# Performance work log

Hardware: AMD Instinct MI355X
Metric: run time of the kernel (lower is better)

## Reference

```python
import jax, jax.numpy as jnp
import numpy as np

N_VERTS = 100000  # number of vertices
N_EDGES = 20000   # number of hyperedges
N_PAIRS = 800000  # (vertex, hyperedge) incidence pairs
DIM = 128
N_LAYERS = 3


def _segment_softmax(vals, seg, num_segments):
    # numerically stable softmax of per-pair values within each segment
    m = jax.ops.segment_max(vals, seg, num_segments=num_segments)
    ex = jnp.exp(vals - m[seg])
    s = jax.ops.segment_sum(ex, seg, num_segments=num_segments)
    return ex / s[seg]


def setup_inputs() -> dict:
    key = jax.random.key(0)
    k1, k2, k3, k4, k5, k6 = jax.random.split(key, 6)
    X = jax.random.normal(k1, (N_VERTS, DIM), dtype=jnp.float32)
    Ws = jax.random.normal(k2, (N_LAYERS, DIM, DIM), dtype=jnp.float32) * 0.05
    bs = jax.random.normal(k3, (N_LAYERS, DIM), dtype=jnp.float32) * 0.05
    e2v_weight = jax.random.uniform(k4, (N_PAIRS,), dtype=jnp.float32)
    pair_v = jax.random.randint(k5, (N_PAIRS,), 0, N_VERTS, dtype=jnp.int32)
    pair_e = jax.random.randint(k6, (N_PAIRS,), 0, N_EDGES, dtype=jnp.int32)
    return {"X": X, "Ws": Ws, "bs": bs, "e2v_weight": e2v_weight,
            "pair_v": pair_v, "pair_e": pair_e}


def reference(X, Ws, bs, e2v_weight, pair_v, pair_e):
    # v2e softmax weights: incidence values are all ones -> softmax per hyperedge
    ones = jnp.ones((pair_e.shape[0],), dtype=X.dtype)
    w_v2e = _segment_softmax(ones, pair_e, N_EDGES)            # [P]
    # e2v softmax weights: softmax of e2v_weight per destination vertex
    w_e2v = _segment_softmax(e2v_weight, pair_v, N_VERTS)      # [P]

    for l in range(N_LAYERS):
        X = X @ Ws[l] + bs[l]                                   # theta
        # v2e: vertex -> hyperedge softmax-weighted aggregation
        Xe = jax.ops.segment_sum(w_v2e[:, None] * X[pair_v], pair_e,
                                 num_segments=N_EDGES)          # [E, D]
        # e2v: hyperedge -> vertex softmax-weighted aggregation
        X = jax.ops.segment_sum(w_e2v[:, None] * Xe[pair_e], pair_v,
                                num_segments=N_VERTS)           # [N, D]
        X = jax.nn.relu(X)                                      # dropout = identity (eval)
    return X
```

## Files before the change

kernel.cpp:

```cpp
#include <hip/hip_runtime.h>
#include <hip/hip_fp16.h>

#define NV 100000
#define NE 20000
#define NP 800000
#define DIM 128
#define NEP 20032

#define EB_SH 7
#define EB 128
#define NBKE ((NE + EB - 1) / EB)
#define ECAP 8192
#define VB_SH 8
#define VB 256
#define NBKV ((NV + VB - 1) / VB)
#define VCAP 3072

#define PPB 8192
#define NPB ((NP + PPB - 1) / PPB)

typedef unsigned short ushort_t;
typedef short bf16x8 __attribute__((ext_vector_type(8)));
typedef float f32x4 __attribute__((ext_vector_type(4)));

__device__ inline unsigned f2bf(float f) {
    unsigned u = __float_as_uint(f);
    return (u + 0x7fffu + ((u >> 16) & 1u)) >> 16;
}
__device__ inline unsigned packbf(float lo, float hi) {
    return f2bf(lo) | (f2bf(hi) << 16);
}
__device__ inline float bflo(unsigned u) { return __uint_as_float(u << 16); }
__device__ inline float bfhi(unsigned u) { return __uint_as_float(u & 0xffff0000u); }


__device__ inline int wave_scan(int v) {
    int lane = threadIdx.x & 63;
#pragma unroll
    for (int off = 1; off < 64; off <<= 1) {
        int u = __shfl_up(v, off, 64);
        if (lane >= off) v += u;
    }
    return v;
}

__global__ __launch_bounds__(256) void k_part(const int* __restrict__ pv,
                                              const int* __restrict__ pe,
                                              const float* __restrict__ ew,
                                              int* __restrict__ gcur_e,
                                              int* __restrict__ gcur_v,
                                              unsigned* __restrict__ stg_e,
                                              uint2* __restrict__ stg_v) {
    __shared__ int he[NBKE], hv[NBKV], be[NBKE], bv[NBKV];
    int t = threadIdx.x;
    for (int b = t; b < NBKE; b += 256) he[b] = 0;
    for (int b = t; b < NBKV; b += 256) hv[b] = 0;
    __syncthreads();

    int blk0 = blockIdx.x * PPB;
    for (int it = 0; it < PPB / 1024; ++it) {
        int base = blk0 + it * 1024 + t * 4;
        if (base + 3 < NP) {
            int4 e4 = *(const int4*)(pe + base);
            int4 v4 = *(const int4*)(pv + base);
            atomicAdd(&he[e4.x >> EB_SH], 1);
            atomicAdd(&he[e4.y >> EB_SH], 1);
            atomicAdd(&he[e4.z >> EB_SH], 1);
            atomicAdd(&he[e4.w >> EB_SH], 1);
            atomicAdd(&hv[v4.x >> VB_SH], 1);
            atomicAdd(&hv[v4.y >> VB_SH], 1);
            atomicAdd(&hv[v4.z >> VB_SH], 1);
            atomicAdd(&hv[v4.w >> VB_SH], 1);
        } else {
            for (int k = 0; k < 4 && base + k < NP; ++k) {
                atomicAdd(&he[pe[base + k] >> EB_SH], 1);
                atomicAdd(&hv[pv[base + k] >> VB_SH], 1);
            }
        }
    }
    __syncthreads();
    for (int b = t; b < NBKE; b += 256) {
        int c = he[b];
        be[b] = c ? atomicAdd(&gcur_e[b], c) : 0;
        he[b] = 0;
    }
    for (int b = t; b < NBKV; b += 256) {
        int c = hv[b];
        bv[b] = c ? atomicAdd(&gcur_v[b], c) : 0;
        hv[b] = 0;
    }
    __syncthreads();
    for (int it = 0; it < PPB / 1024; ++it) {
        int base = blk0 + it * 1024 + t * 4;
        int e[4], v[4];
        float w[4];
        int n = 0;
        if (base + 3 < NP) {
            int4 e4 = *(const int4*)(pe + base);
            int4 v4 = *(const int4*)(pv + base);
            float4 w4 = *(const float4*)(ew + base);
            e[0] = e4.x; e[1] = e4.y; e[2] = e4.z; e[3] = e4.w;
            v[0] = v4.x; v[1] = v4.y; v[2] = v4.z; v[3] = v4.w;
            w[0] = w4.x; w[1] = w4.y; w[2] = w4.z; w[3] = w4.w;
            n = 4;
        } else {
            for (int k = 0; base + k < NP && k < 4; ++k) {
                e[n] = pe[base + k]; v[n] = pv[base + k]; w[n] = ew[base + k]; ++n;
            }
        }
        for (int k = 0; k < n; ++k) {
            int b1 = e[k] >> EB_SH;
            int off = be[b1] + atomicAdd(&he[b1], 1);
            if (off < ECAP) stg_e[(size_t)b1 * ECAP + off] = ((unsigned)v[k] << 15) | (unsigned)e[k];
            int b2 = v[k] >> VB_SH;
            int off2 = bv[b2] + atomicAdd(&hv[b2], 1);
            uint2 rec;
            rec.x = ((unsigned)e[k] << 17) | (unsigned)v[k];
            rec.y = __float_as_uint(expf(w[k]));
            if (off2 < VCAP) stg_v[(size_t)b2 * VCAP + off2] = rec;
        }
    }
}

__global__ __launch_bounds__(256) void scan_buckets(const int* __restrict__ gcur_e,
                                                    const int* __restrict__ gcur_v,
                                                    int* __restrict__ bbase_e,
                                                    int* __restrict__ bbase_v) {
    __shared__ int wsum[5];
    __shared__ int carry;
#pragma unroll
    for (int seg = 0; seg < 2; ++seg) {
        const int* in = seg ? gcur_v : gcur_e;
        int* out = seg ? bbase_v : bbase_e;
        int nb = seg ? NBKV : NBKE;
        if (threadIdx.x == 0) carry = 0;
        __syncthreads();
        for (int base = 0; base < nb; base += 256) {
            int i = base + threadIdx.x;
            int v = (i < nb) ? in[i] : 0;
            int incl = wave_scan(v);
            int wid = threadIdx.x >> 6, lane = threadIdx.x & 63;
            if (lane == 63) wsum[wid] = incl;
            __syncthreads();
            if (threadIdx.x == 0) {
                int run = 0;
#pragma unroll
                for (int j = 0; j < 4; ++j) { int tt = wsum[j]; wsum[j] = run; run += tt; }
                wsum[4] = run;
            }
            __syncthreads();
            if (i < nb) out[i] = incl + wsum[wid] - v + carry;
            __syncthreads();
            if (threadIdx.x == 0) carry += wsum[4];
            __syncthreads();
        }
        if (threadIdx.x == 0) out[nb] = carry;
        __syncthreads();
    }
}

__global__ __launch_bounds__(256) void reorder_e(const unsigned* __restrict__ stg_e,
                                                 const int* __restrict__ gcnt_e,
                                                 const int* __restrict__ bbase_e,
                                                 int* __restrict__ eoff,
                                                 int* __restrict__ eslot_v) {
    __shared__ int hist[EB];
    __shared__ int cur[EB];
    __shared__ int wtot[4];
    __shared__ int data[ECAP];
    int b = blockIdx.x, t = threadIdx.x;
    int lo = b << EB_SH;
    int hi = min(lo + EB, NE);
    int cnt = min(gcnt_e[b], ECAP);
    int base = bbase_e[b];
    if (t < EB) hist[t] = 0;
    __syncthreads();
    const unsigned* stg = stg_e + (size_t)b * ECAP;
    for (int i = t; i < cnt; i += 256) {
        atomicAdd(&hist[(int)(stg[i] & 0x7fffu) - lo], 1);
    }
    __syncthreads();
    int v = (t < EB) ? hist[t] : 0;
    int incl = wave_scan(v);
    int wid = t >> 6, lane = t & 63;
    if (lane == 63) wtot[wid] = incl;
    __syncthreads();
    if (t < EB) {
        int excl = incl - v + (wid == 1 ? wtot[0] : 0);
        cur[t] = excl;
        if (lo + t < hi) eoff[lo + t] = base + excl;
    }
    if (b == NBKE - 1 && t == 0) eoff[NE] = NP;
    __syncthreads();
    for (int i = t; i < cnt; i += 256) {
        unsigned rec = stg[i];
        int e = (int)(rec & 0x7fffu);
        int sl = atomicAdd(&cur[e - lo], 1);
        data[sl] = (int)(rec >> 15);
    }
    __syncthreads();
    for (int i = t; i < cnt; i += 256) eslot_v[base + i] = data[i];
}

__global__ __launch_bounds__(256) void reorder_v(const uint2* __restrict__ stg_v,
                                                 const int* __restrict__ gcnt_v,
                                                 const int* __restrict__ bbase_v,
                                                 int* __restrict__ voff,
                                                 unsigned* __restrict__ vslot) {
    __shared__ int hist[VB];
    __shared__ int cur[VB];
    __shared__ int wtot[4];
    __shared__ unsigned data[VCAP];
    int b = blockIdx.x, t = threadIdx.x;
    int lo = b << VB_SH;
    int hi = min(lo + VB, NV);
    int cnt = min(gcnt_v[b], VCAP);
    int base = bbase_v[b];
    hist[t] = 0;
    __syncthreads();
    const uint2* stg = stg_v + (size_t)b * VCAP;
    for (int i = t; i < cnt; i += 256) {
        atomicAdd(&hist[(int)(stg[i].x & 0x1ffffu) - lo], 1);
    }
    __syncthreads();
    int v = hist[t];
    int incl = wave_scan(v);
    int wid = t >> 6, lane = t & 63;
    if (lane == 63) wtot[wid] = incl;
    __syncthreads();
    int add = 0;
    for (int j = 0; j < wid; ++j) add += wtot[j];
    int excl = incl - v + add;
    cur[t] = excl;
    if (lo + t < hi) voff[lo + t] = base + excl;
    if (b == NBKV - 1 && t == 0) voff[NV] = NP;
    __syncthreads();
    for (int i = t; i < cnt; i += 256) {
        uint2 rec = stg[i];
        int vv = (int)(rec.x & 0x1ffffu);
        int sl = atomicAdd(&cur[vv - lo], 1);
        float w = __uint_as_float(rec.y);
        unsigned hw = (unsigned)__half_as_ushort(__float2half(w));
        data[sl] = (hw << 16) | (rec.x >> 17);
    }
    __syncthreads();
    for (int i = t; i < cnt; i += 256) vslot[base + i] = data[i];
}

__global__ __launch_bounds__(256) void k_cvt(const float* __restrict__ X,
                                             ushort_t* __restrict__ Xbf) {
    int i = blockIdx.x * 256 + threadIdx.x;
    const float4* X4 = (const float4*)X;
    float4 a = X4[(size_t)i * 2];
    float4 b = X4[(size_t)i * 2 + 1];
    uint2 r0, r1;
    r0.x = packbf(a.x, a.y); r0.y = packbf(a.z, a.w);
    r1.x = packbf(b.x, b.y); r1.y = packbf(b.z, b.w);
    ((uint2*)Xbf)[(size_t)i * 2] = r0;
    ((uint2*)Xbf)[(size_t)i * 2 + 1] = r1;
}

__global__ __launch_bounds__(256) void k_cvtW(const float* __restrict__ Ws,
                                              ushort_t* __restrict__ Wt_hi,
                                              ushort_t* __restrict__ Wt_lo) {
    int idx = blockIdx.x * 256 + threadIdx.x;
    int l = idx >> 14;
    int k = (idx >> 7) & 127;
    int c = idx & 127;
    float w = Ws[(size_t)l * 16384 + k * 128 + c];
    unsigned hi = f2bf(w);
    float whi = __uint_as_float(hi << 16);
    unsigned lo = f2bf(w - whi);
    Wt_hi[(size_t)l * 16384 + c * 128 + k] = (ushort_t)hi;
    Wt_lo[(size_t)l * 16384 + c * 128 + k] = (ushort_t)lo;
}


__device__ inline void acc8(float* a, uint4 x) {
    a[0] += bflo(x.x); a[1] += bfhi(x.x);
    a[2] += bflo(x.y); a[3] += bfhi(x.y);
    a[4] += bflo(x.z); a[5] += bfhi(x.z);
    a[6] += bflo(x.w); a[7] += bfhi(x.w);
}

__global__ __launch_bounds__(256) void k_v2e(const ushort_t* __restrict__ Xbf,
                                             const int* __restrict__ eslot_v,
                                             const int* __restrict__ eoff,
                                             ushort_t* __restrict__ Ahi,
                                             ushort_t* __restrict__ Alo) {
    int g = threadIdx.x >> 4;
    int j = threadIdx.x & 15;
    int e = blockIdx.x * 16 + g;
    int s = eoff[e], t = eoff[e + 1];
    const uint4* Xb = (const uint4*)Xbf;
    float a[8] = {0.f, 0.f, 0.f, 0.f, 0.f, 0.f, 0.f, 0.f};
    int i = s;
    for (; i + 4 <= t; i += 4) {
        int v0 = eslot_v[i + 0];
        int v1 = eslot_v[i + 1];
        int v2 = eslot_v[i + 2];
        int v3 = eslot_v[i + 3];
        uint4 x0 = Xb[(size_t)v0 * 16 + j];
        uint4 x1 = Xb[(size_t)v1 * 16 + j];
        uint4 x2 = Xb[(size_t)v2 * 16 + j];
        uint4 x3 = Xb[(size_t)v3 * 16 + j];
        acc8(a, x0); acc8(a, x1); acc8(a, x2); acc8(a, x3);
    }
    for (; i < t; ++i) {
        uint4 x0 = Xb[(size_t)eslot_v[i] * 16 + j];
        acc8(a, x0);
    }
    float inv = (t > s) ? 1.f / (float)(t - s) : 0.f;
#pragma unroll
    for (int k = 0; k < 8; ++k) a[k] *= inv;
    uint4 h;
    h.x = packbf(a[0], a[1]); h.y = packbf(a[2], a[3]);
    h.z = packbf(a[4], a[5]); h.w = packbf(a[6], a[7]);
    float r0 = a[0] - bflo(h.x), r1 = a[1] - bfhi(h.x);
    float r2 = a[2] - bflo(h.y), r3 = a[3] - bfhi(h.y);
    float r4 = a[4] - bflo(h.z), r5 = a[5] - bfhi(h.z);
    float r6 = a[6] - bflo(h.w), r7 = a[7] - bfhi(h.w);
    uint4 lo4;
    lo4.x = packbf(r0, r1); lo4.y = packbf(r2, r3);
    lo4.z = packbf(r4, r5); lo4.w = packbf(r6, r7);
    ((uint4*)Ahi)[(size_t)e * 16 + j] = h;
    ((uint4*)Alo)[(size_t)e * 16 + j] = lo4;
}

__global__ __launch_bounds__(256) void k_gemm(const ushort_t* __restrict__ Ahi,
                                              const ushort_t* __restrict__ Alo,
                                              const ushort_t* __restrict__ Wthi,
                                              const ushort_t* __restrict__ Wtlo,
                                              const float* __restrict__ bvec,
                                              ushort_t* __restrict__ Xe) {
    __shared__ ushort_t lds[4][16][136];
    int wave = threadIdx.x >> 6;
    int l = threadIdx.x & 63;
    int r15 = l & 15;
    int kg = l >> 4;
    int row = blockIdx.x * 64 + wave * 16 + r15;

    bf16x8 ah[4], al[4];
    size_t abase = (size_t)row * 128 + kg * 8;
#pragma unroll
    for (int ks = 0; ks < 4; ++ks) {
        ah[ks] = *(const bf16x8*)(Ahi + abase + ks * 32);
        al[ks] = *(const bf16x8*)(Alo + abase + ks * 32);
    }

#pragma unroll
    for (int ct = 0; ct < 8; ++ct) {
        f32x4 c = {0.f, 0.f, 0.f, 0.f};
        size_t bbase = (size_t)(ct * 16 + r15) * 128 + kg * 8;
#pragma unroll
        for (int ks = 0; ks < 4; ++ks) {
            bf16x8 bh = *(const bf16x8*)(Wthi + bbase + ks * 32);
            bf16x8 bl = *(const bf16x8*)(Wtlo + bbase + ks * 32);
            c = __builtin_amdgcn_mfma_f32_16x16x32_bf16(ah[ks], bh, c, 0, 0, 0);
            c = __builtin_amdgcn_mfma_f32_16x16x32_bf16(ah[ks], bl, c, 0, 0, 0);
            c = __builtin_amdgcn_mfma_f32_16x16x32_bf16(al[ks], bh, c, 0, 0, 0);
        }
        float bias = bvec[ct * 16 + r15];
#pragma unroll
        for (int j = 0; j < 4; ++j) {
            lds[wave][kg * 4 + j][ct * 16 + r15] = (ushort_t)f2bf(c[j] + bias);
        }
    }
    __syncthreads();

    int rrow = l >> 2;
    int piece = l & 3;
    const uint4* src = (const uint4*)((const char*)&lds[wave][0][0] + rrow * 272 + piece * 64);
    int rowg = blockIdx.x * 64 + wave * 16 + rrow;
    if (rowg < NE) {
        int h = piece >> 1;
        ushort_t* dst = Xe + (size_t)h * NEP * 64 + (size_t)rowg * 64 + (piece & 1) * 32;
        uint4* d4 = (uint4*)dst;
        d4[0] = src[0];
        d4[1] = src[1];
        d4[2] = src[2];
        d4[3] = src[3];
    }
}

__global__ __launch_bounds__(256) void k_e2v(const ushort_t* __restrict__ Xe,
                                             const unsigned* __restrict__ vslot,
                                             const int* __restrict__ voff,
                                             float* __restrict__ Xout,
                                             ushort_t* __restrict__ Xbf,
                                             int write_bf) {
    int v = blockIdx.x * 32 + (threadIdx.x >> 3);
    int c8 = threadIdx.x & 7;
    int h = blockIdx.y;
    int s = voff[v], t = voff[v + 1];
    const uint4* base = (const uint4*)(Xe + (size_t)h * NEP * 64);
    float a[8] = {0.f, 0.f, 0.f, 0.f, 0.f, 0.f, 0.f, 0.f};
    float wsum = 0.f;
    int i = s;
    for (; i + 4 <= t; i += 4) {
        unsigned r0 = vslot[i + 0];
        unsigned r1 = vslot[i + 1];
        unsigned r2 = vslot[i + 2];
        unsigned r3 = vslot[i + 3];
        float w0 = __half2float(__ushort_as_half((unsigned short)(r0 >> 16)));
        float w1 = __half2float(__ushort_as_half((unsigned short)(r1 >> 16)));
        float w2 = __half2float(__ushort_as_half((unsigned short)(r2 >> 16)));
        float w3 = __half2float(__ushort_as_half((unsigned short)(r3 >> 16)));
        uint4 x0 = base[(size_t)(r0 & 0xffffu) * 8 + c8];
        uint4 x1 = base[(size_t)(r1 & 0xffffu) * 8 + c8];
        uint4 x2 = base[(size_t)(r2 & 0xffffu) * 8 + c8];
        uint4 x3 = base[(size_t)(r3 & 0xffffu) * 8 + c8];
        wsum += (w0 + w1) + (w2 + w3);
        a[0] = fmaf(w0, bflo(x0.x), a[0]); a[1] = fmaf(w0, bfhi(x0.x), a[1]);
        a[2] = fmaf(w0, bflo(x0.y), a[2]); a[3] = fmaf(w0, bfhi(x0.y), a[3]);
        a[4] = fmaf(w0, bflo(x0.z), a[4]); a[5] = fmaf(w0, bfhi(x0.z), a[5]);
        a[6] = fmaf(w0, bflo(x0.w), a[6]); a[7] = fmaf(w0, bfhi(x0.w), a[7]);
        a[0] = fmaf(w1, bflo(x1.x), a[0]); a[1] = fmaf(w1, bfhi(x1.x), a[1]);
        a[2] = fmaf(w1, bflo(x1.y), a[2]); a[3] = fmaf(w1, bfhi(x1.y), a[3]);
        a[4] = fmaf(w1, bflo(x1.z), a[4]); a[5] = fmaf(w1, bfhi(x1.z), a[5]);
        a[6] = fmaf(w1, bflo(x1.w), a[6]); a[7] = fmaf(w1, bfhi(x1.w), a[7]);
        a[0] = fmaf(w2, bflo(x2.x), a[0]); a[1] = fmaf(w2, bfhi(x2.x), a[1]);
        a[2] = fmaf(w2, bflo(x2.y), a[2]); a[3] = fmaf(w2, bfhi(x2.y), a[3]);
        a[4] = fmaf(w2, bflo(x2.z), a[4]); a[5] = fmaf(w2, bfhi(x2.z), a[5]);
        a[6] = fmaf(w2, bflo(x2.w), a[6]); a[7] = fmaf(w2, bfhi(x2.w), a[7]);
        a[0] = fmaf(w3, bflo(x3.x), a[0]); a[1] = fmaf(w3, bfhi(x3.x), a[1]);
        a[2] = fmaf(w3, bflo(x3.y), a[2]); a[3] = fmaf(w3, bfhi(x3.y), a[3]);
        a[4] = fmaf(w3, bflo(x3.z), a[4]); a[5] = fmaf(w3, bfhi(x3.z), a[5]);
        a[6] = fmaf(w3, bflo(x3.w), a[6]); a[7] = fmaf(w3, bfhi(x3.w), a[7]);
    }
    for (; i < t; ++i) {
        unsigned r0 = vslot[i];
        float w0 = __half2float(__ushort_as_half((unsigned short)(r0 >> 16)));
        uint4 x0 = base[(size_t)(r0 & 0xffffu) * 8 + c8];
        wsum += w0;
        a[0] = fmaf(w0, bflo(x0.x), a[0]); a[1] = fmaf(w0, bfhi(x0.x), a[1]);
        a[2] = fmaf(w0, bflo(x0.y), a[2]); a[3] = fmaf(w0, bfhi(x0.y), a[3]);
        a[4] = fmaf(w0, bflo(x0.z), a[4]); a[5] = fmaf(w0, bfhi(x0.z), a[5]);
        a[6] = fmaf(w0, bflo(x0.w), a[6]); a[7] = fmaf(w0, bfhi(x0.w), a[7]);
    }
    float inv = (wsum > 0.f) ? 1.f / wsum : 0.f;
#pragma unroll
    for (int k = 0; k < 8; ++k) a[k] = fmaxf(a[k] * inv, 0.f);
    if (write_bf) {
        uint4 o;
        o.x = packbf(a[0], a[1]);
        o.y = packbf(a[2], a[3]);
        o.z = packbf(a[4], a[5]);
        o.w = packbf(a[6], a[7]);
        ((uint4*)Xbf)[(size_t)v * 16 + h * 8 + c8] = o;
    } else {
        float4* O = (float4*)Xout;
        O[(size_t)v * 32 + h * 16 + c8 * 2 + 0] = make_float4(a[0], a[1], a[2], a[3]);
        O[(size_t)v * 32 + h * 16 + c8 * 2 + 1] = make_float4(a[4], a[5], a[6], a[7]);
    }
}


extern "C" void kernel_launch(void* const* d_in, const int* in_sizes, int n_in,
                              void* d_out, int out_size, void* d_ws, size_t ws_size,
                              hipStream_t stream) {
    const float* X  = (const float*)d_in[0];
    const float* Ws = (const float*)d_in[1];
    const float* bs = (const float*)d_in[2];
    const float* ew = (const float*)d_in[3];
    const int*   pv = (const int*)d_in[4];
    const int*   pe = (const int*)d_in[5];
    float* Xout = (float*)d_out;

    char* p = (char*)d_ws;
    auto take = [&](size_t bytes) {
        char* q = p;
        p += (bytes + 255) & ~(size_t)255;
        return q;
    };
    ushort_t* Ahi  = (ushort_t*)take((size_t)NEP * DIM * 2);
    ushort_t* Alo  = (ushort_t*)take((size_t)NEP * DIM * 2);
    ushort_t* Xe   = (ushort_t*)take((size_t)2 * NEP * 64 * 2);
    ushort_t* Xbf  = (ushort_t*)take((size_t)NV * DIM * 2);
    ushort_t* Wthi = (ushort_t*)take((size_t)3 * DIM * DIM * 2);
    ushort_t* Wtlo = (ushort_t*)take((size_t)3 * DIM * DIM * 2);
    char* z0 = p;
    int*   gcur_e = (int*)take((size_t)NBKE * 4);
    int*   gcur_v = (int*)take((size_t)NBKV * 4);
    size_t zbytes = (size_t)(p - z0);
    int*      bbase_e = (int*)take((size_t)(NBKE + 1) * 4);
    int*      bbase_v = (int*)take((size_t)(NBKV + 1) * 4);
    int*      eoff    = (int*)take((size_t)(NE + 1) * 4);
    int*      voff    = (int*)take((size_t)(NV + 1) * 4);
    int*      eslot_v = (int*)take((size_t)NP * 4);
    unsigned* vslot   = (unsigned*)take((size_t)NP * 4);
    unsigned* stg_e   = (unsigned*)take((size_t)NBKE * ECAP * 4);
    uint2*    stg_v   = (uint2*)take((size_t)NBKV * VCAP * 8);

    hipMemsetAsync(z0, 0, zbytes, stream);

    k_part<<<NPB, 256, 0, stream>>>(pv, pe, ew, gcur_e, gcur_v, stg_e, stg_v);
    scan_buckets<<<1, 256, 0, stream>>>(gcur_e, gcur_v, bbase_e, bbase_v);
    reorder_e<<<NBKE, 256, 0, stream>>>(stg_e, gcur_e, bbase_e, eoff, eslot_v);
    reorder_v<<<NBKV, 256, 0, stream>>>(stg_v, gcur_v, bbase_v, voff, vslot);
    k_cvt<<<NV * DIM / 8 / 256, 256, 0, stream>>>(X, Xbf);
    k_cvtW<<<3 * DIM * DIM / 256, 256, 0, stream>>>(Ws, Wthi, Wtlo);

    for (int l = 0; l < 3; ++l) {
        k_v2e<<<NE / 16, 256, 0, stream>>>(Xbf, eslot_v, eoff, Ahi, Alo);
        k_gemm<<<NEP / 64, 256, 0, stream>>>(Ahi, Alo,
                                             Wthi + (size_t)l * DIM * DIM,
                                             Wtlo + (size_t)l * DIM * DIM,
                                             bs + (size_t)l * DIM, Xe);
        k_e2v<<<dim3(NV / 32, 2), 256, 0, stream>>>(Xe, vslot, voff, Xout, Xbf,
                                                    (l < 2) ? 1 : 0);
    }
}
```

Baseline: 297.2 us.

## Drop bucket-scan kernel, merge conversion kernels, split v2e edges across half-groups

Removes the single-block bucket scan kernel: each reorder block now sums the preceding bucket counts itself with a block reduction to get its base offset. The X and W conversion kernels are merged into one launch. The v2e gather now gives each hyperedge 32 threads, two half-groups that each take alternate chunks of four incidences and combine through a shuffle, which raises parallelism and memory-level concurrency. The trade-offs are fewer launches and serial steps against redundant per-block prefix reads in the reorder kernels and half the lanes sitting idle during v2e's final store.

After: 292.5 us. About the same (-1.6%).

```diff
diff --git a/kernel.cpp b/kernel.cpp
--- a/kernel.cpp
+++ b/kernel.cpp
@@ -122,59 +122,27 @@
     }
 }
 
-__global__ __launch_bounds__(256) void scan_buckets(const int* __restrict__ gcur_e,
-                                                    const int* __restrict__ gcur_v,
-                                                    int* __restrict__ bbase_e,
-                                                    int* __restrict__ bbase_v) {
-    __shared__ int wsum[5];
-    __shared__ int carry;
-#pragma unroll
-    for (int seg = 0; seg < 2; ++seg) {
-        const int* in = seg ? gcur_v : gcur_e;
-        int* out = seg ? bbase_v : bbase_e;
-        int nb = seg ? NBKV : NBKE;
-        if (threadIdx.x == 0) carry = 0;
-        __syncthreads();
-        for (int base = 0; base < nb; base += 256) {
-            int i = base + threadIdx.x;
-            int v = (i < nb) ? in[i] : 0;
-            int incl = wave_scan(v);
-            int wid = threadIdx.x >> 6, lane = threadIdx.x & 63;
-            if (lane == 63) wsum[wid] = incl;
-            __syncthreads();
-            if (threadIdx.x == 0) {
-                int run = 0;
-#pragma unroll
-                for (int j = 0; j < 4; ++j) { int tt = wsum[j]; wsum[j] = run; run += tt; }
-                wsum[4] = run;
-            }
-            __syncthreads();
-            if (i < nb) out[i] = incl + wsum[wid] - v + carry;
-            __syncthreads();
-            if (threadIdx.x == 0) carry += wsum[4];
-            __syncthreads();
-        }
-        if (threadIdx.x == 0) out[nb] = carry;
-        __syncthreads();
-    }
-}
-
 __global__ __launch_bounds__(256) void reorder_e(const unsigned* __restrict__ stg_e,
                                                  const int* __restrict__ gcnt_e,
-                                                 const int* __restrict__ bbase_e,
                                                  int* __restrict__ eoff,
                                                  int* __restrict__ eslot_v) {
     __shared__ int hist[EB];
     __shared__ int cur[EB];
     __shared__ int wtot[4];
+    __shared__ int red[4];
     __shared__ int data[ECAP];
     int b = blockIdx.x, t = threadIdx.x;
+    int lane = t & 63, wid = t >> 6;
+    int p = (t < b) ? gcnt_e[t] : 0;
+#pragma unroll
+    for (int off = 32; off > 0; off >>= 1) p += __shfl_down(p, off, 64);
+    if (lane == 0) red[wid] = p;
+    if (t < EB) hist[t] = 0;
+    __syncthreads();
+    int base = red[0] + red[1] + red[2] + red[3];
     int lo = b << EB_SH;
     int hi = min(lo + EB, NE);
     int cnt = min(gcnt_e[b], ECAP);
-    int base = bbase_e[b];
-    if (t < EB) hist[t] = 0;
-    __syncthreads();
     const unsigned* stg = stg_e + (size_t)b * ECAP;
     for (int i = t; i < cnt; i += 256) {
         atomicAdd(&hist[(int)(stg[i] & 0x7fffu) - lo], 1);
@@ -182,7 +150,6 @@
     __syncthreads();
     int v = (t < EB) ? hist[t] : 0;
     int incl = wave_scan(v);
-    int wid = t >> 6, lane = t & 63;
     if (lane == 63) wtot[wid] = incl;
     __syncthreads();
     if (t < EB) {
@@ -204,20 +171,27 @@
 
 __global__ __launch_bounds__(256) void reorder_v(const uint2* __restrict__ stg_v,
                                                  const int* __restrict__ gcnt_v,
-                                                 const int* __restrict__ bbase_v,
                                                  int* __restrict__ voff,
                                                  unsigned* __restrict__ vslot) {
     __shared__ int hist[VB];
     __shared__ int cur[VB];
     __shared__ int wtot[4];
+    __shared__ int red[4];
     __shared__ unsigned data[VCAP];
     int b = blockIdx.x, t = threadIdx.x;
+    int lane = t & 63, wid = t >> 6;
+    int p = 0;
+    if (t < b) p += gcnt_v[t];
+    if (t + 256 < b) p += gcnt_v[t + 256];
+#pragma unroll
+    for (int off = 32; off > 0; off >>= 1) p += __shfl_down(p, off, 64);
+    if (lane == 0) red[wid] = p;
+    hist[t] = 0;
+    __syncthreads();
+    int base = red[0] + red[1] + red[2] + red[3];
     int lo = b << VB_SH;
     int hi = min(lo + VB, NV);
     int cnt = min(gcnt_v[b], VCAP);
-    int base = bbase_v[b];
-    hist[t] = 0;
-    __syncthreads();
     const uint2* stg = stg_v + (size_t)b * VCAP;
     for (int i = t; i < cnt; i += 256) {
         atomicAdd(&hist[(int)(stg[i].x & 0x1ffffu) - lo], 1);
@@ -225,7 +199,6 @@
     __syncthreads();
     int v = hist[t];
     int incl = wave_scan(v);
-    int wid = t >> 6, lane = t & 63;
     if (lane == 63) wtot[wid] = incl;
     __syncthreads();
     int add = 0;
@@ -247,32 +220,35 @@
     for (int i = t; i < cnt; i += 256) vslot[base + i] = data[i];
 }
 
-__global__ __launch_bounds__(256) void k_cvt(const float* __restrict__ X,
-                                             ushort_t* __restrict__ Xbf) {
-    int i = blockIdx.x * 256 + threadIdx.x;
-    const float4* X4 = (const float4*)X;
-    float4 a = X4[(size_t)i * 2];
-    float4 b = X4[(size_t)i * 2 + 1];
-    uint2 r0, r1;
-    r0.x = packbf(a.x, a.y); r0.y = packbf(a.z, a.w);
-    r1.x = packbf(b.x, b.y); r1.y = packbf(b.z, b.w);
-    ((uint2*)Xbf)[(size_t)i * 2] = r0;
-    ((uint2*)Xbf)[(size_t)i * 2 + 1] = r1;
-}
-
-__global__ __launch_bounds__(256) void k_cvtW(const float* __restrict__ Ws,
-                                              ushort_t* __restrict__ Wt_hi,
-                                              ushort_t* __restrict__ Wt_lo) {
-    int idx = blockIdx.x * 256 + threadIdx.x;
-    int l = idx >> 14;
-    int k = (idx >> 7) & 127;
-    int c = idx & 127;
-    float w = Ws[(size_t)l * 16384 + k * 128 + c];
-    unsigned hi = f2bf(w);
-    float whi = __uint_as_float(hi << 16);
-    unsigned lo = f2bf(w - whi);
-    Wt_hi[(size_t)l * 16384 + c * 128 + k] = (ushort_t)hi;
-    Wt_lo[(size_t)l * 16384 + c * 128 + k] = (ushort_t)lo;
+#define XB (NV * DIM / 8 / 256)
+#define WB (3 * DIM * DIM / 256)
+__global__ __launch_bounds__(256) void k_cvtall(const float* __restrict__ X,
+                                                ushort_t* __restrict__ Xbf,
+                                                const float* __restrict__ Ws,
+                                                ushort_t* __restrict__ Wt_hi,
+                                                ushort_t* __restrict__ Wt_lo) {
+    if (blockIdx.x < XB) {
+        int i = blockIdx.x * 256 + threadIdx.x;
+        const float4* X4 = (const float4*)X;
+        float4 a = X4[(size_t)i * 2];
+        float4 b = X4[(size_t)i * 2 + 1];
+        uint2 r0, r1;
+        r0.x = packbf(a.x, a.y); r0.y = packbf(a.z, a.w);
+        r1.x = packbf(b.x, b.y); r1.y = packbf(b.z, b.w);
+        ((uint2*)Xbf)[(size_t)i * 2] = r0;
+        ((uint2*)Xbf)[(size_t)i * 2 + 1] = r1;
+    } else {
+        int idx = (blockIdx.x - XB) * 256 + threadIdx.x;
+        int l = idx >> 14;
+        int k = (idx >> 7) & 127;
+        int c = idx & 127;
+        float w = Ws[(size_t)l * 16384 + k * 128 + c];
+        unsigned hi = f2bf(w);
+        float whi = __uint_as_float(hi << 16);
+        unsigned lo = f2bf(w - whi);
+        Wt_hi[(size_t)l * 16384 + c * 128 + k] = (ushort_t)hi;
+        Wt_lo[(size_t)l * 16384 + c * 128 + k] = (ushort_t)lo;
+    }
 }
 
 
@@ -288,14 +264,15 @@
                                              const int* __restrict__ eoff,
                                              ushort_t* __restrict__ Ahi,
                                              ushort_t* __restrict__ Alo) {
-    int g = threadIdx.x >> 4;
+    int g = threadIdx.x >> 5;
+    int half = (threadIdx.x >> 4) & 1;
     int j = threadIdx.x & 15;
-    int e = blockIdx.x * 16 + g;
+    int e = blockIdx.x * 8 + g;
     int s = eoff[e], t = eoff[e + 1];
     const uint4* Xb = (const uint4*)Xbf;
     float a[8] = {0.f, 0.f, 0.f, 0.f, 0.f, 0.f, 0.f, 0.f};
-    int i = s;
-    for (; i + 4 <= t; i += 4) {
+    int i = s + half * 4;
+    for (; i + 4 <= t; i += 8) {
         int v0 = eslot_v[i + 0];
         int v1 = eslot_v[i + 1];
         int v2 = eslot_v[i + 2];
@@ -306,25 +283,29 @@
         uint4 x3 = Xb[(size_t)v3 * 16 + j];
         acc8(a, x0); acc8(a, x1); acc8(a, x2); acc8(a, x3);
     }
-    for (; i < t; ++i) {
-        uint4 x0 = Xb[(size_t)eslot_v[i] * 16 + j];
+    for (int k = i; k < t && k < i + 4; ++k) {
+        uint4 x0 = Xb[(size_t)eslot_v[k] * 16 + j];
         acc8(a, x0);
     }
-    float inv = (t > s) ? 1.f / (float)(t - s) : 0.f;
-#pragma unroll
-    for (int k = 0; k < 8; ++k) a[k] *= inv;
-    uint4 h;
-    h.x = packbf(a[0], a[1]); h.y = packbf(a[2], a[3]);
-    h.z = packbf(a[4], a[5]); h.w = packbf(a[6], a[7]);
-    float r0 = a[0] - bflo(h.x), r1 = a[1] - bfhi(h.x);
-    float r2 = a[2] - bflo(h.y), r3 = a[3] - bfhi(h.y);
-    float r4 = a[4] - bflo(h.z), r5 = a[5] - bfhi(h.z);
-    float r6 = a[6] - bflo(h.w), r7 = a[7] - bfhi(h.w);
-    uint4 lo4;
-    lo4.x = packbf(r0, r1); lo4.y = packbf(r2, r3);
-    lo4.z = packbf(r4, r5); lo4.w = packbf(r6, r7);
-    ((uint4*)Ahi)[(size_t)e * 16 + j] = h;
-    ((uint4*)Alo)[(size_t)e * 16 + j] = lo4;
+#pragma unroll
+    for (int k = 0; k < 8; ++k) a[k] += __shfl_xor(a[k], 16, 64);
+    if (half == 0) {
+        float inv = (t > s) ? 1.f / (float)(t - s) : 0.f;
+#pragma unroll
+        for (int k = 0; k < 8; ++k) a[k] *= inv;
+        uint4 h;
+        h.x = packbf(a[0], a[1]); h.y = packbf(a[2], a[3]);
+        h.z = packbf(a[4], a[5]); h.w = packbf(a[6], a[7]);
+        float r0 = a[0] - bflo(h.x), r1 = a[1] - bfhi(h.x);
+        float r2 = a[2] - bflo(h.y), r3 = a[3] - bfhi(h.y);
+        float r4 = a[4] - bflo(h.z), r5 = a[5] - bfhi(h.z);
+        float r6 = a[6] - bflo(h.w), r7 = a[7] - bfhi(h.w);
+        uint4 lo4;
+        lo4.x = packbf(r0, r1); lo4.y = packbf(r2, r3);
+        lo4.z = packbf(r4, r5); lo4.w = packbf(r6, r7);
+        ((uint4*)Ahi)[(size_t)e * 16 + j] = h;
+        ((uint4*)Alo)[(size_t)e * 16 + j] = lo4;
+    }
 }
 
 __global__ __launch_bounds__(256) void k_gemm(const ushort_t* __restrict__ Ahi,
@@ -483,8 +464,6 @@
     int*   gcur_e = (int*)take((size_t)NBKE * 4);
     int*   gcur_v = (int*)take((size_t)NBKV * 4);
     size_t zbytes = (size_t)(p - z0);
-    int*      bbase_e = (int*)take((size_t)(NBKE + 1) * 4);
-    int*      bbase_v = (int*)take((size_t)(NBKV + 1) * 4);
     int*      eoff    = (int*)take((size_t)(NE + 1) * 4);
     int*      voff    = (int*)take((size_t)(NV + 1) * 4);
     int*      eslot_v = (int*)take((size_t)NP * 4);
@@ -495,14 +474,12 @@
     hipMemsetAsync(z0, 0, zbytes, stream);
 
     k_part<<<NPB, 256, 0, stream>>>(pv, pe, ew, gcur_e, gcur_v, stg_e, stg_v);
-    scan_buckets<<<1, 256, 0, stream>>>(gcur_e, gcur_v, bbase_e, bbase_v);
-    reorder_e<<<NBKE, 256, 0, stream>>>(stg_e, gcur_e, bbase_e, eoff, eslot_v);
-    reorder_v<<<NBKV, 256, 0, stream>>>(stg_v, gcur_v, bbase_v, voff, vslot);
-    k_cvt<<<NV * DIM / 8 / 256, 256, 0, stream>>>(X, Xbf);
-    k_cvtW<<<3 * DIM * DIM / 256, 256, 0, stream>>>(Ws, Wthi, Wtlo);
+    reorder_e<<<NBKE, 256, 0, stream>>>(stg_e, gcur_e, eoff, eslot_v);
+    reorder_v<<<NBKV, 256, 0, stream>>>(stg_v, gcur_v, voff, vslot);
+    k_cvtall<<<XB + WB, 256, 0, stream>>>(X, Xbf, Ws, Wthi, Wtlo);
 
     for (int l = 0; l < 3; ++l) {
-        k_v2e<<<NE / 16, 256, 0, stream>>>(Xbf, eslot_v, eoff, Ahi, Alo);
+        k_v2e<<<NE / 8, 256, 0, stream>>>(Xbf, eslot_v, eoff, Ahi, Alo);
         k_gemm<<<NEP / 64, 256, 0, stream>>>(Ahi, Alo,
                                              Wthi + (size_t)l * DIM * DIM,
                                              Wtlo + (size_t)l * DIM * DIM,
```
